# Kernel tuning notes

Measured on AMD Instinct MI355X. Metric: run time of the kernel, lower is better.

The kernel has to match this reference:

```python
import jax, jax.numpy as jnp
import numpy as np

K = 3  # number of SGC propagation hops


def setup_inputs() -> dict:
    key = jax.random.key(0)
    k1, k2, k3 = jax.random.split(key, 3)
    N, E, F = 50000, 800000, 128
    x = jax.random.normal(k1, (N, F), dtype=jnp.float32)
    edge_index = jax.random.randint(k2, (2, E), 0, N, dtype=jnp.int64)
    weight = jax.random.normal(k3, (F, 1), dtype=jnp.float32) * (1.0 / np.sqrt(F))
    bias = jnp.zeros((1,), dtype=jnp.float32)
    return {"x": x, "edge_index": edge_index, "weight": weight, "bias": bias}


def reference(x, edge_index, weight, bias):
    N = x.shape[0]
    # gcn_norm: add self-loops, symmetric normalization D^-1/2 (A+I) D^-1/2
    loops = jnp.arange(N, dtype=edge_index.dtype)
    src = jnp.concatenate([edge_index[0], loops])  # message sources
    dst = jnp.concatenate([edge_index[1], loops])  # aggregation targets
    ones = jnp.ones(src.shape[0], dtype=x.dtype)
    deg = jax.ops.segment_sum(ones, dst, num_segments=N)  # [N]
    dinv = jnp.where(deg > 0, jax.lax.rsqrt(deg), 0.0)
    norm = (dinv[src] * dinv[dst])[:, None]  # [E+N, 1]
    # K hops of S @ x
    for _ in range(K):
        x = jax.ops.segment_sum(norm * x[src], dst, num_segments=N)
    out = x @ weight + bias  # [N, 1]
    return jnp.square(out)
```

## Files before the change

### kernel.cpp

```cpp
#include <hip/hip_runtime.h>

#define FEAT 128
#define NPB 128
#define NPB_SHIFT 7
#define SBITS 25
#define SMASK ((1u << SBITS) - 1u)
#define NSCAT 256
#define CAPB 64
#define CAPB_SHIFT 6
#define NGEMV 256
#define NBMAX 2048
#define TPB 256

__global__ void k1_scat_gemv(const float* __restrict__ x, const int* __restrict__ src,
                             const int* __restrict__ dst, const float* __restrict__ w,
                             int N, int E, int NB, int chunk,
                             unsigned* __restrict__ ebuf, unsigned char* __restrict__ cnt2,
                             float* __restrict__ z) {
    const int b = blockIdx.x;
    const int t = threadIdx.x;
    if (b < NSCAT) {
        __shared__ int h[NBMAX];
        const int k = b;
        int beg = k * chunk;
        int end = min(E, beg + chunk);
        for (int i = t; i < NB; i += TPB) h[i] = 0;
        __syncthreads();
        for (int e = beg + t; e < end; e += TPB) {
            int s = src[e], d = dst[e];
            int bk = d >> NPB_SHIFT;
            int l = atomicAdd(&h[bk], 1);
            if (l < CAPB)
                ebuf[((size_t)(bk * NSCAT + k) << CAPB_SHIFT) + l] =
                    ((unsigned)(d & (NPB - 1)) << SBITS) | (unsigned)s;
        }
        __syncthreads();
        for (int i = t; i < NB; i += TPB)
            cnt2[(size_t)i * NSCAT + k] = (unsigned char)min(h[i], CAPB);
    } else {
        int gb  = b - NSCAT;
        int hw  = t >> 5;
        int l32 = t & 31;
        float4 wv = ((const float4*)w)[l32];
        for (int node = gb * 8 + hw; node < N; node += NGEMV * 8) {
            float4 xv = ((const float4*)(x + (size_t)node * FEAT))[l32];
            float s = xv.x * wv.x + xv.y * wv.y + xv.z * wv.z + xv.w * wv.w;
            #pragma unroll
            for (int o = 16; o >= 1; o >>= 1) s += __shfl_xor(s, o, 64);
            if (l32 == 0) z[node] = s;
        }
    }
}

__global__ void k2_deg_u0(const unsigned* __restrict__ ebuf,
                          const unsigned char* __restrict__ cnt2,
                          const float* __restrict__ z,
                          float* __restrict__ dinv, float* __restrict__ u0, int N) {
    __shared__ int cdeg[NPB];
    const int b = blockIdx.x;
    const int t = threadIdx.x;
    if (t < NPB) cdeg[t] = 0;
    __syncthreads();
    {
        int cnt = cnt2[(size_t)b * NSCAT + t];
        const unsigned* cell = ebuf + ((size_t)(b * NSCAT + t) << CAPB_SHIFT);
        for (int j = 0; j < cnt; ++j)
            atomicAdd(&cdeg[cell[j] >> SBITS], 1);
    }
    __syncthreads();
    if (t < NPB) {
        int node = (b << NPB_SHIFT) + t;
        if (node < N) {
            float dv = 1.0f / sqrtf(1.0f + (float)cdeg[t]);
            dinv[node] = dv;
            u0[node]   = dv * z[node];
        }
    }
}

template <bool LAST>
__global__ void k3_hop(const unsigned* __restrict__ ebuf,
                       const unsigned char* __restrict__ cnt2,
                       const float* __restrict__ dinv, const float* __restrict__ uin,
                       float* __restrict__ uout, const float* __restrict__ bias, int N) {
    __shared__ float acc[NPB];
    const int b = blockIdx.x;
    const int t = threadIdx.x;
    if (t < NPB) acc[t] = 0.0f;
    __syncthreads();
    {
        int cnt = cnt2[(size_t)b * NSCAT + t];
        const unsigned* cell = ebuf + ((size_t)(b * NSCAT + t) << CAPB_SHIFT);
        for (int j = 0; j < cnt; ++j) {
            unsigned p = cell[j];
            atomicAdd(&acc[p >> SBITS], uin[p & SMASK]);
        }
    }
    __syncthreads();
    if (t < NPB) {
        int node = (b << NPB_SHIFT) + t;
        if (node < N) {
            float d = dinv[node];
            float sum = acc[t] + uin[node];
            if (LAST) { float v = d * sum + bias[0]; uout[node] = v * v; }
            else      { uout[node] = d * d * sum; }
        }
    }
}

__global__ void f_init_deg(float* __restrict__ deg, int N) {
    int i = blockIdx.x * blockDim.x + threadIdx.x;
    if (i < N) deg[i] = 1.0f;
}
__global__ void f_count_deg(const int* __restrict__ dst, float* __restrict__ deg, int E) {
    int e = blockIdx.x * blockDim.x + threadIdx.x;
    if (e < E) unsafeAtomicAdd(&deg[dst[e]], 1.0f);
}
__global__ void f_dot_dinv(const float* __restrict__ x, const float* __restrict__ w,
                           const float* __restrict__ deg, float* __restrict__ dinv,
                           float* __restrict__ z, int N) {
    int wid  = (blockIdx.x * blockDim.x + threadIdx.x) >> 6;
    int lane = threadIdx.x & 63;
    if (wid >= N) return;
    const float2* xr = reinterpret_cast<const float2*>(x + (size_t)wid * FEAT);
    const float2* wr = reinterpret_cast<const float2*>(w);
    float2 xv = xr[lane];
    float2 wv = wr[lane];
    float s = xv.x * wv.x + xv.y * wv.y;
    #pragma unroll
    for (int o = 32; o >= 1; o >>= 1) s += __shfl_xor(s, o, 64);
    if (lane == 0) { z[wid] = s; dinv[wid] = 1.0f / sqrtf(deg[wid]); }
}
__global__ void f_hop_self(const float* __restrict__ za, const float* __restrict__ dinv,
                           float* __restrict__ zb, int N) {
    int i = blockIdx.x * blockDim.x + threadIdx.x;
    if (i < N) { float d = dinv[i]; zb[i] = d * d * za[i]; }
}
__global__ void f_hop_edges(const int* __restrict__ src, const int* __restrict__ dst,
                            const float* __restrict__ za, const float* __restrict__ dinv,
                            float* __restrict__ zb, int E) {
    int e = blockIdx.x * blockDim.x + threadIdx.x;
    if (e < E) {
        int s = src[e], d = dst[e];
        unsafeAtomicAdd(&zb[d], dinv[s] * dinv[d] * za[s]);
    }
}
__global__ void f_final(const float* __restrict__ z, const float* __restrict__ bias,
                        float* __restrict__ out, int N) {
    int i = blockIdx.x * blockDim.x + threadIdx.x;
    if (i < N) { float v = z[i] + bias[0]; out[i] = v * v; }
}

extern "C" void kernel_launch(void* const* d_in, const int* in_sizes, int n_in,
                              void* d_out, int out_size, void* d_ws, size_t ws_size,
                              hipStream_t stream) {
    const float* x    = (const float*)d_in[0];
    const int*   ei   = (const int*)d_in[1];
    const float* w    = (const float*)d_in[2];
    const float* bias = (const float*)d_in[3];
    float*       out  = (float*)d_out;

    const int N = in_sizes[0] / FEAT;
    const int E = in_sizes[1] / 2;
    const int* src = ei;
    const int* dst = ei + E;

    const int NB = (N + NPB - 1) >> NPB_SHIFT;

    size_t ebuf_elems = (size_t)NB * NSCAT * CAPB;
    size_t off_z    = ebuf_elems * sizeof(unsigned);
    size_t off_cnt2 = off_z + (size_t)4 * N * sizeof(float);
    size_t need     = off_cnt2 + (size_t)NB * NSCAT + 256;

    bool fast = (NB <= NBMAX) && (N <= (1 << SBITS)) &&
                ((size_t)E * 4 <= (size_t)NB * NSCAT * CAPB) &&
                (ws_size >= need);

    if (fast) {
        unsigned*      ebuf = (unsigned*)d_ws;
        float*         z    = (float*)((char*)d_ws + off_z);
        float*         dinv = z + N;
        float*         ua   = dinv + N;
        float*         ub   = ua + N;
        unsigned char* cnt2 = (unsigned char*)((char*)d_ws + off_cnt2);

        const int chunk = (E + NSCAT - 1) / NSCAT;

        k1_scat_gemv<<<NSCAT + NGEMV, TPB, 0, stream>>>(x, src, dst, w, N, E, NB, chunk,
                                                        ebuf, cnt2, z);
        k2_deg_u0<<<NB, TPB, 0, stream>>>(ebuf, cnt2, z, dinv, ua, N);
        k3_hop<false><<<NB, TPB, 0, stream>>>(ebuf, cnt2, dinv, ua, ub, bias, N);
        k3_hop<false><<<NB, TPB, 0, stream>>>(ebuf, cnt2, dinv, ub, ua, bias, N);
        k3_hop<true ><<<NB, TPB, 0, stream>>>(ebuf, cnt2, dinv, ua, out, bias, N);
    } else {
        float* deg  = (float*)d_ws;
        float* dinv = deg;
        float* z0   = deg + N;
        float* z1   = z0 + N;
        const int B = 256;
        const int gN = (N + B - 1) / B;
        const int gE = (E + B - 1) / B;
        const int gW = (N * 64 + B - 1) / B;
        f_init_deg<<<gN, B, 0, stream>>>(deg, N);
        f_count_deg<<<gE, B, 0, stream>>>(dst, deg, E);
        f_dot_dinv<<<gW, B, 0, stream>>>(x, w, deg, dinv, z0, N);
        f_hop_self<<<gN, B, 0, stream>>>(z0, dinv, z1, N);
        f_hop_edges<<<gE, B, 0, stream>>>(src, dst, z0, dinv, z1, E);
        f_hop_self<<<gN, B, 0, stream>>>(z1, dinv, z0, N);
        f_hop_edges<<<gE, B, 0, stream>>>(src, dst, z1, dinv, z0, E);
        f_hop_self<<<gN, B, 0, stream>>>(z0, dinv, z1, N);
        f_hop_edges<<<gE, B, 0, stream>>>(src, dst, z0, dinv, z1, E);
        f_final<<<gN, B, 0, stream>>>(z1, bias, out, N);
    }
}
```

Baseline: 51.79 us.

## Fuse degree and three hop kernels into one persistent kernel with grid barriers

The degree/u0 kernel and the three hop kernels are merged into one kernel. Blocks synchronise between phases with a global atomic-counter barrier, which k1 resets. Separate u0/u1/u2 buffers are used so no phase overwrites data another block may still read, and intermediate results are written with relaxed agent-scope atomic stores. This removes three kernel launch boundaries and their drain/refill gaps. In exchange it relies on all blocks being co-resident, and it uses relaxed ordering without explicit acquire/release fences, which is a memory-visibility risk.

```diff
diff --git a/kernel.cpp b/kernel.cpp
--- a/kernel.cpp
+++ b/kernel.cpp
@@ -9,16 +9,31 @@
 #define CAPB 64
 #define CAPB_SHIFT 6
 #define NGEMV 256
-#define NBMAX 2048
+#define NBMAX 1024
 #define TPB 256
+
+__device__ __forceinline__ void astore_f(float* p, float v) {
+    __hip_atomic_store(p, v, __ATOMIC_RELAXED, __HIP_MEMORY_SCOPE_AGENT);
+}
+
+__device__ __forceinline__ void gsync(int* bar, int target) {
+    __syncthreads();
+    if (threadIdx.x == 0) {
+        __hip_atomic_fetch_add(bar, 1, __ATOMIC_RELAXED, __HIP_MEMORY_SCOPE_AGENT);
+        while (__hip_atomic_load(bar, __ATOMIC_RELAXED, __HIP_MEMORY_SCOPE_AGENT) < target)
+            __builtin_amdgcn_s_sleep(4);
+    }
+    __syncthreads();
+}
 
 __global__ void k1_scat_gemv(const float* __restrict__ x, const int* __restrict__ src,
                              const int* __restrict__ dst, const float* __restrict__ w,
                              int N, int E, int NB, int chunk,
                              unsigned* __restrict__ ebuf, unsigned char* __restrict__ cnt2,
-                             float* __restrict__ z) {
+                             float* __restrict__ z, int* __restrict__ bar) {
     const int b = blockIdx.x;
     const int t = threadIdx.x;
+    if (b == 0 && t == 0) *bar = 0;
     if (b < NSCAT) {
         __shared__ int h[NBMAX];
         const int k = b;
@@ -52,40 +67,14 @@
     }
 }
 
-__global__ void k2_deg_u0(const unsigned* __restrict__ ebuf,
-                          const unsigned char* __restrict__ cnt2,
-                          const float* __restrict__ z,
-                          float* __restrict__ dinv, float* __restrict__ u0, int N) {
-    __shared__ int cdeg[NPB];
-    const int b = blockIdx.x;
-    const int t = threadIdx.x;
-    if (t < NPB) cdeg[t] = 0;
-    __syncthreads();
-    {
-        int cnt = cnt2[(size_t)b * NSCAT + t];
-        const unsigned* cell = ebuf + ((size_t)(b * NSCAT + t) << CAPB_SHIFT);
-        for (int j = 0; j < cnt; ++j)
-            atomicAdd(&cdeg[cell[j] >> SBITS], 1);
-    }
-    __syncthreads();
-    if (t < NPB) {
-        int node = (b << NPB_SHIFT) + t;
-        if (node < N) {
-            float dv = 1.0f / sqrtf(1.0f + (float)cdeg[t]);
-            dinv[node] = dv;
-            u0[node]   = dv * z[node];
-        }
-    }
-}
-
 template <bool LAST>
-__global__ void k3_hop(const unsigned* __restrict__ ebuf,
-                       const unsigned char* __restrict__ cnt2,
-                       const float* __restrict__ dinv, const float* __restrict__ uin,
-                       float* __restrict__ uout, const float* __restrict__ bias, int N) {
-    __shared__ float acc[NPB];
-    const int b = blockIdx.x;
-    const int t = threadIdx.x;
+__device__ __forceinline__ void hop_phase(const unsigned* __restrict__ ebuf,
+                                          const unsigned char* __restrict__ cnt2,
+                                          const float* __restrict__ dinv,
+                                          const float* __restrict__ uin,
+                                          float* __restrict__ uout,
+                                          const float* __restrict__ bias,
+                                          int N, int b, int t, float* acc) {
     if (t < NPB) acc[t] = 0.0f;
     __syncthreads();
     {
@@ -103,9 +92,47 @@
             float d = dinv[node];
             float sum = acc[t] + uin[node];
             if (LAST) { float v = d * sum + bias[0]; uout[node] = v * v; }
-            else      { uout[node] = d * d * sum; }
-        }
-    }
+            else      { astore_f(&uout[node], d * d * sum); }
+        }
+    }
+}
+
+__global__ void __launch_bounds__(TPB, 4) k2_fused(
+    const unsigned* __restrict__ ebuf, const unsigned char* __restrict__ cnt2,
+    const float* __restrict__ z, const float* __restrict__ bias,
+    float* __restrict__ dinv, float* __restrict__ u0, float* __restrict__ u1,
+    float* __restrict__ u2, float* __restrict__ out, int* __restrict__ bar,
+    int N, int NB)
+{
+    __shared__ int   cdeg[NPB];
+    __shared__ float acc[NPB];
+    const int b = blockIdx.x;
+    const int t = threadIdx.x;
+
+    if (t < NPB) cdeg[t] = 0;
+    __syncthreads();
+    {
+        int cnt = cnt2[(size_t)b * NSCAT + t];
+        const unsigned* cell = ebuf + ((size_t)(b * NSCAT + t) << CAPB_SHIFT);
+        for (int j = 0; j < cnt; ++j)
+            atomicAdd(&cdeg[cell[j] >> SBITS], 1);
+    }
+    __syncthreads();
+    if (t < NPB) {
+        int node = (b << NPB_SHIFT) + t;
+        if (node < N) {
+            float dv = 1.0f / sqrtf(1.0f + (float)cdeg[t]);
+            astore_f(&dinv[node], dv);
+            astore_f(&u0[node], dv * z[node]);
+        }
+    }
+    gsync(bar, NB);
+
+    hop_phase<false>(ebuf, cnt2, dinv, u0, u1, bias, N, b, t, acc);
+    gsync(bar, 2 * NB);
+    hop_phase<false>(ebuf, cnt2, dinv, u1, u2, bias, N, b, t, acc);
+    gsync(bar, 3 * NB);
+    hop_phase<true >(ebuf, cnt2, dinv, u2, out, bias, N, b, t, acc);
 }
 
 __global__ void f_init_deg(float* __restrict__ deg, int N) {
@@ -169,7 +196,8 @@
 
     size_t ebuf_elems = (size_t)NB * NSCAT * CAPB;
     size_t off_z    = ebuf_elems * sizeof(unsigned);
-    size_t off_cnt2 = off_z + (size_t)4 * N * sizeof(float);
+    size_t off_bar  = (off_z + (size_t)5 * N * sizeof(float) + 255) & ~(size_t)255;
+    size_t off_cnt2 = off_bar + 256;
     size_t need     = off_cnt2 + (size_t)NB * NSCAT + 256;
 
     bool fast = (NB <= NBMAX) && (N <= (1 << SBITS)) &&
@@ -180,18 +208,18 @@
         unsigned*      ebuf = (unsigned*)d_ws;
         float*         z    = (float*)((char*)d_ws + off_z);
         float*         dinv = z + N;
-        float*         ua   = dinv + N;
-        float*         ub   = ua + N;
+        float*         u0   = dinv + N;
+        float*         u1   = u0 + N;
+        float*         u2   = u1 + N;
+        int*           bar  = (int*)((char*)d_ws + off_bar);
         unsigned char* cnt2 = (unsigned char*)((char*)d_ws + off_cnt2);
 
         const int chunk = (E + NSCAT - 1) / NSCAT;
 
         k1_scat_gemv<<<NSCAT + NGEMV, TPB, 0, stream>>>(x, src, dst, w, N, E, NB, chunk,
-                                                        ebuf, cnt2, z);
-        k2_deg_u0<<<NB, TPB, 0, stream>>>(ebuf, cnt2, z, dinv, ua, N);
-        k3_hop<false><<<NB, TPB, 0, stream>>>(ebuf, cnt2, dinv, ua, ub, bias, N);
-        k3_hop<false><<<NB, TPB, 0, stream>>>(ebuf, cnt2, dinv, ub, ua, bias, N);
-        k3_hop<true ><<<NB, TPB, 0, stream>>>(ebuf, cnt2, dinv, ua, out, bias, N);
+                                                        ebuf, cnt2, z, bar);
+        k2_fused<<<NB, TPB, 0, stream>>>(ebuf, cnt2, z, bias, dinv, u0, u1, u2, out, bar,
+                                         N, NB);
     } else {
         float* deg  = (float*)d_ws;
         float* dinv = deg;
```

Result: slower. 104.8 us (+102.4%).

## Fuse degree and three hops into one persistent kernel with grid barriers

Applied to the files above, without the earlier changes.

Replaces the degree kernel and three per-hop kernels with one persistent kernel. Node blocks shrink to 98 so that about 511 blocks plus one coordinator block can be co-resident, and the blocks synchronise through a flag-based software grid barrier. Each block compacts its scattered edge cells into a contiguous per-block list using a prefix scan, and keeps dinv and its own node values in LDS. This removes three launch gaps and the repeated scans of the sparse 256-cell layout, at the cost of spin-wait barriers, a possible deadlock if not all blocks are resident, and integer division in the scatter.

```diff
diff --git a/kernel.cpp b/kernel.cpp
--- a/kernel.cpp
+++ b/kernel.cpp
@@ -1,16 +1,37 @@
 #include <hip/hip_runtime.h>
 
 #define FEAT 128
-#define NPB 128
-#define NPB_SHIFT 7
+#define NPB 98
 #define SBITS 25
 #define SMASK ((1u << SBITS) - 1u)
 #define NSCAT 256
-#define CAPB 64
-#define CAPB_SHIFT 6
+#define CAPB 32
+#define CAPB_SHIFT 5
+#define CAP2 4096
+#define CAP2_SHIFT 12
 #define NGEMV 256
-#define NBMAX 2048
 #define TPB 256
+#define LINE 32
+#define NBHIST 512
+
+__device__ __forceinline__ void astore_f(float* p, float v) {
+    __hip_atomic_store(p, v, __ATOMIC_RELAXED, __HIP_MEMORY_SCOPE_AGENT);
+}
+__device__ __forceinline__ void astore_i(int* p, int v) {
+    __hip_atomic_store(p, v, __ATOMIC_RELAXED, __HIP_MEMORY_SCOPE_AGENT);
+}
+__device__ __forceinline__ int aload_i(const int* p) {
+    return __hip_atomic_load(p, __ATOMIC_RELAXED, __HIP_MEMORY_SCOPE_AGENT);
+}
+
+__device__ __forceinline__ void wbar(int* arr, int* flags, int b, int ep) {
+    __syncthreads();
+    if (threadIdx.x == 0) {
+        astore_i(&arr[b], ep);
+        while (aload_i(&flags[b * LINE]) < ep) __builtin_amdgcn_s_sleep(1);
+    }
+    __syncthreads();
+}
 
 __global__ void k1_scat_gemv(const float* __restrict__ x, const int* __restrict__ src,
                              const int* __restrict__ dst, const float* __restrict__ w,
@@ -20,23 +41,23 @@
     const int b = blockIdx.x;
     const int t = threadIdx.x;
     if (b < NSCAT) {
-        __shared__ int h[NBMAX];
-        const int k = b;
-        int beg = k * chunk;
-        int end = min(E, beg + chunk);
+        __shared__ int h[NBHIST];
         for (int i = t; i < NB; i += TPB) h[i] = 0;
         __syncthreads();
+        int beg = b * chunk;
+        int end = min(E, beg + chunk);
         for (int e = beg + t; e < end; e += TPB) {
             int s = src[e], d = dst[e];
-            int bk = d >> NPB_SHIFT;
+            int bk  = (int)((unsigned)d / NPB);
+            int loc = d - bk * NPB;
             int l = atomicAdd(&h[bk], 1);
             if (l < CAPB)
-                ebuf[((size_t)(bk * NSCAT + k) << CAPB_SHIFT) + l] =
-                    ((unsigned)(d & (NPB - 1)) << SBITS) | (unsigned)s;
+                ebuf[((size_t)(bk * NSCAT + b) << CAPB_SHIFT) + l] =
+                    ((unsigned)loc << SBITS) | (unsigned)s;
         }
         __syncthreads();
         for (int i = t; i < NB; i += TPB)
-            cnt2[(size_t)i * NSCAT + k] = (unsigned char)min(h[i], CAPB);
+            cnt2[(size_t)i * NSCAT + b] = (unsigned char)min(h[i], CAPB);
     } else {
         int gb  = b - NSCAT;
         int hw  = t >> 5;
@@ -52,60 +73,120 @@
     }
 }
 
-__global__ void k2_deg_u0(const unsigned* __restrict__ ebuf,
-                          const unsigned char* __restrict__ cnt2,
-                          const float* __restrict__ z,
-                          float* __restrict__ dinv, float* __restrict__ u0, int N) {
-    __shared__ int cdeg[NPB];
+__global__ void __launch_bounds__(TPB, 2) k2_fused(
+    const unsigned* __restrict__ ebuf, const unsigned char* __restrict__ cnt2,
+    const float* __restrict__ z, const float* __restrict__ bias,
+    unsigned* __restrict__ ebuf2,
+    float* __restrict__ u0, float* __restrict__ u1, float* __restrict__ u2,
+    float* __restrict__ out, int* __restrict__ arr, int* __restrict__ flags,
+    int N, int NB)
+{
     const int b = blockIdx.x;
     const int t = threadIdx.x;
-    if (t < NPB) cdeg[t] = 0;
-    __syncthreads();
+
+    if (b == NB) {
+        for (int ep = 1; ep <= 3; ++ep) {
+            for (;;) {
+                int ok = 1;
+                for (int i = t; i < NB; i += TPB)
+                    if (aload_i(&arr[i]) < ep) { ok = 0; break; }
+                if (__syncthreads_and(ok)) break;
+                __builtin_amdgcn_s_sleep(2);
+            }
+            for (int i = t; i < NB; i += TPB)
+                astore_i(&flags[i * LINE], ep);
+        }
+        return;
+    }
+
+    __shared__ float uown[NPB], dinvL[NPB], acc[NPB];
+    __shared__ int   degL[NPB];
+    __shared__ int   pref[TPB];
+    __shared__ int   cntB_s;
+    const int base = b * NPB;
+    const int nn   = min(NPB, N - base);
+
+    if (t < NPB) degL[t] = 0;
+    __syncthreads();
+    int cnt = cnt2[(size_t)b * NSCAT + t];
+    pref[t] = cnt;
+    __syncthreads();
+    #pragma unroll
+    for (int off = 1; off < TPB; off <<= 1) {
+        int v = (t >= off) ? pref[t - off] : 0;
+        __syncthreads();
+        pref[t] += v;
+        __syncthreads();
+    }
+    int mypos = pref[t] - cnt;
+    if (t == TPB - 1) cntB_s = min(pref[t], CAP2);
     {
-        int cnt = cnt2[(size_t)b * NSCAT + t];
         const unsigned* cell = ebuf + ((size_t)(b * NSCAT + t) << CAPB_SHIFT);
-        for (int j = 0; j < cnt; ++j)
-            atomicAdd(&cdeg[cell[j] >> SBITS], 1);
-    }
-    __syncthreads();
-    if (t < NPB) {
-        int node = (b << NPB_SHIFT) + t;
-        if (node < N) {
-            float dv = 1.0f / sqrtf(1.0f + (float)cdeg[t]);
-            dinv[node] = dv;
-            u0[node]   = dv * z[node];
-        }
-    }
-}
-
-template <bool LAST>
-__global__ void k3_hop(const unsigned* __restrict__ ebuf,
-                       const unsigned char* __restrict__ cnt2,
-                       const float* __restrict__ dinv, const float* __restrict__ uin,
-                       float* __restrict__ uout, const float* __restrict__ bias, int N) {
-    __shared__ float acc[NPB];
-    const int b = blockIdx.x;
-    const int t = threadIdx.x;
-    if (t < NPB) acc[t] = 0.0f;
-    __syncthreads();
-    {
-        int cnt = cnt2[(size_t)b * NSCAT + t];
-        const unsigned* cell = ebuf + ((size_t)(b * NSCAT + t) << CAPB_SHIFT);
+        unsigned* dst2 = ebuf2 + ((size_t)b << CAP2_SHIFT);
+        #pragma unroll 4
         for (int j = 0; j < cnt; ++j) {
             unsigned p = cell[j];
-            atomicAdd(&acc[p >> SBITS], uin[p & SMASK]);
+            atomicAdd(&degL[p >> SBITS], 1);
+            int pos = mypos + j;
+            if (pos < CAP2) dst2[pos] = p;
         }
     }
     __syncthreads();
-    if (t < NPB) {
-        int node = (b << NPB_SHIFT) + t;
-        if (node < N) {
-            float d = dinv[node];
-            float sum = acc[t] + uin[node];
-            if (LAST) { float v = d * sum + bias[0]; uout[node] = v * v; }
-            else      { uout[node] = d * d * sum; }
-        }
-    }
+    if (t < nn) {
+        float dv = 1.0f / sqrtf(1.0f + (float)degL[t]);
+        dinvL[t] = dv;
+        float u = dv * z[base + t];
+        uown[t] = u;
+        astore_f(&u0[base + t], u);
+    }
+    wbar(arr, flags, b, 1);
+
+    const unsigned* dst2 = ebuf2 + ((size_t)b << CAP2_SHIFT);
+    const int cntB = cntB_s;
+
+    if (t < NPB) acc[t] = 0.0f;
+    __syncthreads();
+    for (int j = t; j < cntB; j += TPB) {
+        unsigned p = dst2[j];
+        atomicAdd(&acc[p >> SBITS], u0[p & SMASK]);
+    }
+    __syncthreads();
+    if (t < nn) {
+        float dv = dinvL[t];
+        float nu = dv * dv * (acc[t] + uown[t]);
+        uown[t] = nu;
+        astore_f(&u1[base + t], nu);
+    }
+    wbar(arr, flags, b, 2);
+
+    if (t < NPB) acc[t] = 0.0f;
+    __syncthreads();
+    for (int j = t; j < cntB; j += TPB) {
+        unsigned p = dst2[j];
+        atomicAdd(&acc[p >> SBITS], u1[p & SMASK]);
+    }
+    __syncthreads();
+    if (t < nn) {
+        float dv = dinvL[t];
+        float nu = dv * dv * (acc[t] + uown[t]);
+        uown[t] = nu;
+        astore_f(&u2[base + t], nu);
+    }
+    wbar(arr, flags, b, 3);
+
+    if (t < NPB) acc[t] = 0.0f;
+    __syncthreads();
+    for (int j = t; j < cntB; j += TPB) {
+        unsigned p = dst2[j];
+        atomicAdd(&acc[p >> SBITS], u2[p & SMASK]);
+    }
+    __syncthreads();
+    if (t < nn) {
+        float dv = dinvL[t];
+        float v = dv * (acc[t] + uown[t]) + bias[0];
+        out[base + t] = v * v;
+    }
+    if (t == 0) { astore_i(&arr[b], 0); astore_i(&flags[b * LINE], 0); }
 }
 
 __global__ void f_init_deg(float* __restrict__ deg, int N) {
@@ -165,33 +246,39 @@
     const int* src = ei;
     const int* dst = ei + E;
 
-    const int NB = (N + NPB - 1) >> NPB_SHIFT;
-
-    size_t ebuf_elems = (size_t)NB * NSCAT * CAPB;
-    size_t off_z    = ebuf_elems * sizeof(unsigned);
-    size_t off_cnt2 = off_z + (size_t)4 * N * sizeof(float);
-    size_t need     = off_cnt2 + (size_t)NB * NSCAT + 256;
-
-    bool fast = (NB <= NBMAX) && (N <= (1 << SBITS)) &&
-                ((size_t)E * 4 <= (size_t)NB * NSCAT * CAPB) &&
+    const int NB = (N + NPB - 1) / NPB;
+
+    size_t ebuf_b  = (size_t)NB * NSCAT * CAPB * sizeof(unsigned);
+    size_t ebuf2_b = (size_t)NB * CAP2 * sizeof(unsigned);
+    size_t off_e2    = ebuf_b;
+    size_t off_z     = off_e2 + ebuf2_b;
+    size_t off_arr   = (off_z + (size_t)4 * N * sizeof(float) + 255) & ~(size_t)255;
+    size_t off_flags = (off_arr + (size_t)NB * sizeof(int) + 255) & ~(size_t)255;
+    size_t off_cnt2  = off_flags + (size_t)NB * LINE * sizeof(int);
+    size_t need      = off_cnt2 + (size_t)NB * NSCAT + 256;
+
+    bool fast = (NB + 1 <= 512) && (N <= (1 << SBITS)) &&
+                ((size_t)E <= (size_t)8 * NB * NSCAT) &&
+                ((size_t)E * 2 <= (size_t)NB * CAP2) &&
                 (ws_size >= need);
 
     if (fast) {
-        unsigned*      ebuf = (unsigned*)d_ws;
-        float*         z    = (float*)((char*)d_ws + off_z);
-        float*         dinv = z + N;
-        float*         ua   = dinv + N;
-        float*         ub   = ua + N;
-        unsigned char* cnt2 = (unsigned char*)((char*)d_ws + off_cnt2);
+        unsigned*      ebuf  = (unsigned*)d_ws;
+        unsigned*      ebuf2 = (unsigned*)((char*)d_ws + off_e2);
+        float*         z     = (float*)((char*)d_ws + off_z);
+        float*         u0    = z + N;
+        float*         u1    = u0 + N;
+        float*         u2    = u1 + N;
+        int*           arr   = (int*)((char*)d_ws + off_arr);
+        int*           flags = (int*)((char*)d_ws + off_flags);
+        unsigned char* cnt2  = (unsigned char*)((char*)d_ws + off_cnt2);
 
         const int chunk = (E + NSCAT - 1) / NSCAT;
 
-        k1_scat_gemv<<<NSCAT + NGEMV, TPB, 0, stream>>>(x, src, dst, w, N, E, NB, chunk,
-                                                        ebuf, cnt2, z);
-        k2_deg_u0<<<NB, TPB, 0, stream>>>(ebuf, cnt2, z, dinv, ua, N);
-        k3_hop<false><<<NB, TPB, 0, stream>>>(ebuf, cnt2, dinv, ua, ub, bias, N);
-        k3_hop<false><<<NB, TPB, 0, stream>>>(ebuf, cnt2, dinv, ub, ua, bias, N);
-        k3_hop<true ><<<NB, TPB, 0, stream>>>(ebuf, cnt2, dinv, ua, out, bias, N);
+        k1_scat_gemv<<<NSCAT + NGEMV, TPB, 0, stream>>>(x, src, dst, w, N, E, NB,
+                                                        chunk, ebuf, cnt2, z);
+        k2_fused<<<NB + 1, TPB, 0, stream>>>(ebuf, cnt2, z, bias, ebuf2,
+                                             u0, u1, u2, out, arr, flags, N, NB);
     } else {
         float* deg  = (float*)d_ws;
         float* dinv = deg;
```

Measured after the change: 53.24 us. +2.8%, slower.
